# Kernel tuning notes

Hardware: AMD Instinct MI355X
Metric: run time of the kernel (lower is better)

The kernel has to match this reference:

```python
import jax, jax.numpy as jnp
import numpy as np

EMBED_DIM = 1024
NUM_HEADS = 16
HEAD_DIM = EMBED_DIM // NUM_HEADS
SEQ_LEN = 2048
B = 2


def setup_inputs() -> dict:
    key = jax.random.key(0)
    ks = jax.random.split(key, 6)
    x = jax.random.normal(ks[0], (B, SEQ_LEN, EMBED_DIM), dtype=jnp.float32)
    # Linear params (torch Linear: y = x @ W.T + b); store W as [in, out] for einsum
    qkv_w = jax.random.normal(ks[1], (EMBED_DIM, 3 * EMBED_DIM), dtype=jnp.float32) * (EMBED_DIM ** -0.5)
    qkv_b = jnp.zeros((3 * EMBED_DIM,), dtype=jnp.float32)
    proj_w = jax.random.normal(ks[2], (EMBED_DIM, EMBED_DIM), dtype=jnp.float32) * (EMBED_DIM ** -0.5)
    proj_b = jnp.zeros((EMBED_DIM,), dtype=jnp.float32)
    # relative position bias table [2L-1, H], trunc_normal std=0.02 ~ normal*0.02
    bias_table = jax.random.normal(ks[3], (2 * SEQ_LEN - 1, NUM_HEADS), dtype=jnp.float32) * 0.02
    return {"x": x, "qkv_w": qkv_w, "qkv_b": qkv_b, "proj_w": proj_w, "proj_b": proj_b, "bias_table": bias_table}


def _rel_pos_index(L):
    coords = jnp.arange(L)
    return (coords[None, :] - coords[:, None]) + (SEQ_LEN - 1)  # [L, L] int


def reference(x, qkv_w, qkv_b, proj_w, proj_b, bias_table):
    Bsz, L, C = x.shape
    scale = HEAD_DIM ** -0.5
    qkv = x @ qkv_w + qkv_b                               # [B, L, 3C]
    qkv = qkv.reshape(Bsz, L, 3, NUM_HEADS, HEAD_DIM)
    q = jnp.transpose(qkv[:, :, 0], (0, 2, 1, 3))          # [B, H, L, D]
    k = jnp.transpose(qkv[:, :, 1], (0, 2, 1, 3))
    v = jnp.transpose(qkv[:, :, 2], (0, 2, 1, 3))
    attn = jnp.einsum('bhqd,bhkd->bhqk', q, k) * scale     # [B, H, L, L]
    rel_bias = bias_table[_rel_pos_index(L)]               # [L, L, H]
    attn = attn + jnp.transpose(rel_bias, (2, 0, 1))[None]  # broadcast over batch
    attn = jax.nn.softmax(attn, axis=-1)
    out = jnp.einsum('bhqk,bhkd->bhqd', attn, v)           # [B, H, L, D]
    out = jnp.transpose(out, (0, 2, 1, 3)).reshape(Bsz, L, C)
    return out @ proj_w + proj_b
```

## Files before the change

kernel.cpp:

```cpp
#include <hip/hip_runtime.h>

typedef short bf16x4 __attribute__((ext_vector_type(4)));
typedef short bf16x8 __attribute__((ext_vector_type(8)));
typedef float f32x4 __attribute__((ext_vector_type(4)));
typedef float f32x16 __attribute__((ext_vector_type(16)));

__device__ __forceinline__ unsigned short f2bf(float f) {
  union { float f; unsigned int u; } v; v.f = f;
  unsigned int r = v.u + 0x7FFFu + ((v.u >> 16) & 1u);
  return (unsigned short)(r >> 16);
}

__device__ __forceinline__ float exp2_fast(float x) {
  float r;
  asm("v_exp_f32 %0, %1" : "=v"(r) : "v"(x));
  return r;
}

__device__ __forceinline__ unsigned int cvt_pk_bf16(float lo, float hi) {
  unsigned int r;
  asm("v_cvt_pk_bf16_f32 %0, %1, %2" : "=v"(r) : "v"(lo), "v"(hi));
  return r;
}


__global__ __launch_bounds__(256) void k_convert_x(const float4* __restrict__ in,
                                                   ushort4* __restrict__ out) {
  int id = blockIdx.x * 256 + threadIdx.x;
  float4 v = in[id];
  ushort4 o;
  o.x = f2bf(v.x); o.y = f2bf(v.y); o.z = f2bf(v.z); o.w = f2bf(v.w);
  out[id] = o;
}

__global__ __launch_bounds__(256) void k_transpose_bf16(const float* __restrict__ in,
                                                        unsigned short* __restrict__ out,
                                                        int R, int C) {
  __shared__ float tile[32][33];
  int tx = threadIdx.x, ty = threadIdx.y;
  int c0 = blockIdx.x * 32, r0 = blockIdx.y * 32;
#pragma unroll
  for (int i = 0; i < 32; i += 8) tile[ty + i][tx] = in[(size_t)(r0 + ty + i) * C + c0 + tx];
  __syncthreads();
#pragma unroll
  for (int i = 0; i < 32; i += 8) out[(size_t)(c0 + ty + i) * R + r0 + tx] = f2bf(tile[tx][ty + i]);
}

__global__ __launch_bounds__(256) void k_bias_cols(const float* __restrict__ bt,
                                                   float* __restrict__ bh) {
  int i = blockIdx.x * 256 + threadIdx.x;
  if (i < 4095 * 16) bh[(i & 15) * 4096 + (i >> 4)] = bt[i] * 1.44269504089f;
}

template <int EPI>
__global__ __launch_bounds__(512) void k_gemm(const unsigned short* __restrict__ A,
                                              const unsigned short* __restrict__ Bt,
                                              const float* __restrict__ bias,
                                              float* __restrict__ Cf,
                                              unsigned short* __restrict__ qb,
                                              unsigned short* __restrict__ kb,
                                              unsigned short* __restrict__ vtb) {
  __shared__ unsigned short Alds[2][128 * 64];
  __shared__ unsigned short Blds[2][128 * 64];
  const int t = threadIdx.x;
  const int l = t & 63, w = t >> 6;
  const int l15 = l & 15, l4 = l >> 4;
  const int wm = w >> 2, wn = w & 3;

  const int hwid = blockIdx.x;
  const int x = hwid & 7, loc = hwid >> 3;
  const int bm = ((x >> 1) * 8 + (loc & 7)) * 128;
  const int bn = ((x & 1) * (EPI ? 12 : 4) + (loc >> 3)) * 128;

  const int srow = t >> 3;
  const int sc = t & 7;
  const unsigned short* agl = A + (size_t)(bm + srow) * 1024 + sc * 8;
  const unsigned short* bgl = Bt + (size_t)(bn + srow) * 1024 + sc * 8;
  const int wls = srow * 64 + ((sc ^ (srow & 7)) * 8);

  f32x4 acc[4][2];
#pragma unroll
  for (int i = 0; i < 4; ++i)
#pragma unroll
    for (int j = 0; j < 2; ++j) acc[i][j] = (f32x4){0.f, 0.f, 0.f, 0.f};

  bf16x8 ra[4], rb[4];

#define GLOAD(REGS, KT)                                                       \
  _Pragma("unroll") for (int q = 0; q < 2; ++q) {                             \
    REGS[q] = *(const bf16x8*)(agl + (size_t)q * 65536 + (KT) * 64);          \
    REGS[2 + q] = *(const bf16x8*)(bgl + (size_t)q * 65536 + (KT) * 64);      \
  }
#define SWRITE(REGS, CUR)                                                     \
  _Pragma("unroll") for (int q = 0; q < 2; ++q) {                             \
    *(bf16x8*)&Alds[CUR][q * 4096 + wls] = REGS[q];                           \
    *(bf16x8*)&Blds[CUR][q * 4096 + wls] = REGS[2 + q];                       \
  }

  GLOAD(ra, 0);
  GLOAD(rb, 1);
  SWRITE(ra, 0);
  asm volatile("s_waitcnt lgkmcnt(0)" ::: "memory");
  __builtin_amdgcn_s_barrier();

#define GEMM_PHASE(KT, RFREE, RPEND)                                          \
  {                                                                           \
    const int cur_ = (KT) & 1;                                                \
    if ((KT) + 2 < 16) { GLOAD(RFREE, (KT) + 2); }                            \
    __builtin_amdgcn_s_setprio(1);                                            \
    _Pragma("unroll") for (int kc = 0; kc < 2; ++kc) {                        \
      bf16x8 af[4], bv[2];                                                    \
      _Pragma("unroll") for (int i = 0; i < 4; ++i) {                         \
        int ra_ = wm * 64 + i * 16 + l15;                                     \
        af[i] = *(const bf16x8*)&Alds[cur_][ra_ * 64 +                        \
                                            (((kc * 4 + l4) ^ (l15 & 7))) * 8]; \
      }                                                                       \
      _Pragma("unroll") for (int j = 0; j < 2; ++j) {                         \
        int rb_ = wn * 32 + j * 16 + l15;                                     \
        bv[j] = *(const bf16x8*)&Blds[cur_][rb_ * 64 +                        \
                                            (((kc * 4 + l4) ^ (l15 & 7))) * 8]; \
      }                                                                       \
      _Pragma("unroll") for (int i = 0; i < 4; ++i)                           \
        _Pragma("unroll") for (int jn = 0; jn < 2; ++jn)                      \
          acc[i][jn] =                                                        \
              __builtin_amdgcn_mfma_f32_16x16x32_bf16(af[i], bv[jn],          \
                                                      acc[i][jn], 0, 0, 0);   \
    }                                                                         \
    __builtin_amdgcn_s_setprio(0);                                            \
    if ((KT) + 1 < 16) { SWRITE(RPEND, cur_ ^ 1); }                           \
    asm volatile("s_waitcnt lgkmcnt(0)" ::: "memory");                        \
    __builtin_amdgcn_s_barrier();                                             \
  }

  for (int kt = 0; kt < 16; kt += 2) {
    GEMM_PHASE(kt, ra, rb);
    GEMM_PHASE(kt + 1, rb, ra);
  }
#undef GEMM_PHASE
#undef SWRITE
#undef GLOAD

#pragma unroll
  for (int i = 0; i < 4; ++i) {
#pragma unroll
    for (int jn = 0; jn < 2; ++jn) {
      int n = bn + wn * 32 + jn * 16 + l15;
      float bval = bias[n];
#pragma unroll
      for (int j = 0; j < 4; ++j) {
        int m = bm + wm * 64 + i * 16 + l4 * 4 + j;
        float v = acc[i][jn][j] + bval;
        if (EPI == 0) {
          Cf[(size_t)m * 1024 + n] = v;
        } else {
          int which = n >> 10, hh = (n >> 6) & 15, d = n & 63;
          int bb = m >> 11, pos = m & 2047;
          int bhh = bb * 16 + hh;
          if (which == 0)
            qb[((size_t)bhh * 2048 + pos) * 64 + d] = f2bf(v * 0.18033688f);
          else if (which == 1)
            kb[((size_t)bhh * 2048 + pos) * 64 + d] = f2bf(v);
          else
            vtb[((size_t)bhh * 64 + d) * 2048 + pos] = f2bf(v);
        }
      }
    }
  }
}

__global__ __launch_bounds__(256) void k_attn(const unsigned short* __restrict__ qbuf,
                                              const unsigned short* __restrict__ kbuf,
                                              const unsigned short* __restrict__ vtbuf,
                                              const float* __restrict__ biash,
                                              unsigned short* __restrict__ aout) {
  __shared__ __align__(16) unsigned short Klds[2][64 * 64];
  __shared__ __align__(16) unsigned short Vlds[2][64 * 64];

  const int t = threadIdx.x;
  const int w = t >> 6, l = t & 63;
  const int l31 = l & 31, hi = l >> 5;

  const int bid = blockIdx.x;
  const int swzb = (bid & 7) * 64 + (bid >> 3);
  const int qt = swzb & 15;
  const int bh = swzb >> 4;
  const int h = bh & 15, b = bh >> 4;
  const int qbase = qt * 128;
  const int wq = qbase + w * 32;

  bf16x8 qB[4];
  {
    const unsigned short* qrow = qbuf + ((size_t)bh * 2048 + wq + l31) * 64;
#pragma unroll
    for (int ds = 0; ds < 4; ++ds) qB[ds] = *(const bf16x8*)&qrow[ds * 16 + hi * 8];
  }

  f32x16 O[2];
#pragma unroll
  for (int i = 0; i < 16; ++i) { O[0][i] = 0.f; O[1][i] = 0.f; }
  float m_run = -3e38f, l_run = 0.f;

  const int c0r = t >> 3, c0c = t & 7;
  const unsigned short* kg = kbuf + ((size_t)bh * 2048 + c0r) * 64 + c0c * 8;
  const unsigned short* vg = vtbuf + ((size_t)bh * 64 + c0r) * 2048 + c0c * 8;
  const int wKV = c0r * 64 + ((c0c ^ (c0r & 7)) * 8);

  {
    bf16x8 k0 = *(const bf16x8*)(kg);
    bf16x8 k1 = *(const bf16x8*)(kg + 32 * 64);
    bf16x8 v0 = *(const bf16x8*)(vg);
    bf16x8 v1 = *(const bf16x8*)(vg + 32 * 2048);
    *(bf16x8*)&Klds[0][wKV] = k0;
    *(bf16x8*)&Klds[0][wKV + 2048] = k1;
    *(bf16x8*)&Vlds[0][wKV] = v0;
    *(bf16x8*)&Vlds[0][wKV + 2048] = v1;
  }
  __syncthreads();

  const float* bgl = biash + h * 4096 + 2047 - (wq + l31) + 4 * hi;

  for (int kt = 0; kt < 32; ++kt) {
    const int cur = kt & 1;

    bf16x8 kst0, kst1, vst0, vst1;
    if (kt < 31) {
      const unsigned short* kga = kg + (size_t)(kt + 1) * 4096;
      const unsigned short* vga = vg + (kt + 1) * 64;
      kst0 = *(const bf16x8*)(kga);
      kst1 = *(const bf16x8*)(kga + 32 * 64);
      vst0 = *(const bf16x8*)(vga);
      vst1 = *(const bf16x8*)(vga + 32 * 2048);
    }
    const int kbase = kt * 64;

    f32x4 bq[2][4];
#pragma unroll
    for (int kt2 = 0; kt2 < 2; ++kt2)
#pragma unroll
      for (int g = 0; g < 4; ++g)
        __builtin_memcpy(&bq[kt2][g], &bgl[kbase + 32 * kt2 + 8 * g], 16);

    f32x16 sacc[2];
#pragma unroll
    for (int i = 0; i < 16; ++i) { sacc[0][i] = 0.f; sacc[1][i] = 0.f; }
    __builtin_amdgcn_s_setprio(1);
#pragma unroll
    for (int kt2 = 0; kt2 < 2; ++kt2) {
      int row = kt2 * 32 + l31;
      int rsw = row & 7;
#pragma unroll
      for (int ds = 0; ds < 4; ++ds) {
        bf16x8 ka = *(const bf16x8*)&Klds[cur][row * 64 + (((2 * ds + hi) ^ rsw) * 8)];
        sacc[kt2] = __builtin_amdgcn_mfma_f32_32x32x16_bf16(ka, qB[ds], sacc[kt2], 0, 0, 0);
      }
    }
    __builtin_amdgcn_s_setprio(0);

#pragma unroll
    for (int kt2 = 0; kt2 < 2; ++kt2)
#pragma unroll
      for (int g = 0; g < 4; ++g)
#pragma unroll
        for (int r = 0; r < 4; ++r) sacc[kt2][4 * g + r] += bq[kt2][g][r];

    float mx;
    {
      float q0 = fmaxf(fmaxf(sacc[0][0], sacc[0][1]), fmaxf(sacc[0][2], sacc[0][3]));
      float q1 = fmaxf(fmaxf(sacc[0][4], sacc[0][5]), fmaxf(sacc[0][6], sacc[0][7]));
      float q2 = fmaxf(fmaxf(sacc[0][8], sacc[0][9]), fmaxf(sacc[0][10], sacc[0][11]));
      float q3 = fmaxf(fmaxf(sacc[0][12], sacc[0][13]), fmaxf(sacc[0][14], sacc[0][15]));
      float q4 = fmaxf(fmaxf(sacc[1][0], sacc[1][1]), fmaxf(sacc[1][2], sacc[1][3]));
      float q5 = fmaxf(fmaxf(sacc[1][4], sacc[1][5]), fmaxf(sacc[1][6], sacc[1][7]));
      float q6 = fmaxf(fmaxf(sacc[1][8], sacc[1][9]), fmaxf(sacc[1][10], sacc[1][11]));
      float q7 = fmaxf(fmaxf(sacc[1][12], sacc[1][13]), fmaxf(sacc[1][14], sacc[1][15]));
      mx = fmaxf(fmaxf(fmaxf(q0, q1), fmaxf(q2, q3)), fmaxf(fmaxf(q4, q5), fmaxf(q6, q7)));
      mx = fmaxf(mx, __shfl_xor(mx, 32));
    }

    if (__any(mx > m_run + 8.f)) {
      float mnew = fmaxf(m_run, mx);
      float alpha = exp2_fast(m_run - mnew);
      m_run = mnew;
      l_run *= alpha;
#pragma unroll
      for (int g = 0; g < 4; ++g)
#pragma unroll
        for (int r = 0; r < 4; ++r) {
          float a_lo = __shfl(alpha, 8 * g + r);
          float a_hi = __shfl(alpha, 8 * g + r + 4);
          float aq = hi ? a_hi : a_lo;
          O[0][4 * g + r] *= aq;
          O[1][4 * g + r] *= aq;
        }
    }

#pragma unroll
    for (int kt2 = 0; kt2 < 2; ++kt2)
#pragma unroll
      for (int i = 0; i < 16; ++i) sacc[kt2][i] = exp2_fast(sacc[kt2][i] - m_run);
    {
      float s0 = (sacc[0][0] + sacc[0][1]) + (sacc[0][2] + sacc[0][3]);
      float s1 = (sacc[0][4] + sacc[0][5]) + (sacc[0][6] + sacc[0][7]);
      float s2 = (sacc[0][8] + sacc[0][9]) + (sacc[0][10] + sacc[0][11]);
      float s3 = (sacc[0][12] + sacc[0][13]) + (sacc[0][14] + sacc[0][15]);
      float s4 = (sacc[1][0] + sacc[1][1]) + (sacc[1][2] + sacc[1][3]);
      float s5 = (sacc[1][4] + sacc[1][5]) + (sacc[1][6] + sacc[1][7]);
      float s6 = (sacc[1][8] + sacc[1][9]) + (sacc[1][10] + sacc[1][11]);
      float s7 = (sacc[1][12] + sacc[1][13]) + (sacc[1][14] + sacc[1][15]);
      float rs = ((s0 + s1) + (s2 + s3)) + ((s4 + s5) + (s6 + s7));
      rs += __shfl_xor(rs, 32);
      l_run += rs;
    }

    bf16x8 pa[2][2];
#pragma unroll
    for (int kt2 = 0; kt2 < 2; ++kt2)
#pragma unroll
      for (int mm = 0; mm < 2; ++mm) {
        union { unsigned int u[4]; bf16x8 v; } pk;
        pk.u[0] = cvt_pk_bf16(sacc[kt2][8 * mm + 0], sacc[kt2][8 * mm + 1]);
        pk.u[1] = cvt_pk_bf16(sacc[kt2][8 * mm + 2], sacc[kt2][8 * mm + 3]);
        pk.u[2] = cvt_pk_bf16(sacc[kt2][8 * mm + 4], sacc[kt2][8 * mm + 5]);
        pk.u[3] = cvt_pk_bf16(sacc[kt2][8 * mm + 6], sacc[kt2][8 * mm + 7]);
        pa[kt2][mm] = pk.v;
      }

    __builtin_amdgcn_s_setprio(1);
#pragma unroll
    for (int dt = 0; dt < 2; ++dt) {
      int row = dt * 32 + l31;
      int rsw = row & 7;
#pragma unroll
      for (int kt2 = 0; kt2 < 2; ++kt2)
#pragma unroll
        for (int mm = 0; mm < 2; ++mm) {
          int cA = (4 * kt2 + 2 * mm) ^ rsw;
          int cB = (4 * kt2 + 2 * mm + 1) ^ rsw;
          bf16x4 vlo = *(const bf16x4*)&Vlds[cur][row * 64 + cA * 8 + 4 * hi];
          bf16x4 vhi = *(const bf16x4*)&Vlds[cur][row * 64 + cB * 8 + 4 * hi];
          bf16x8 vb = __builtin_shufflevector(vlo, vhi, 0, 1, 2, 3, 4, 5, 6, 7);
          O[dt] = __builtin_amdgcn_mfma_f32_32x32x16_bf16(pa[kt2][mm], vb, O[dt], 0, 0, 0);
        }
    }
    __builtin_amdgcn_s_setprio(0);

    if (kt < 31) {
      *(bf16x8*)&Klds[cur ^ 1][wKV] = kst0;
      *(bf16x8*)&Klds[cur ^ 1][wKV + 2048] = kst1;
      *(bf16x8*)&Vlds[cur ^ 1][wKV] = vst0;
      *(bf16x8*)&Vlds[cur ^ 1][wKV + 2048] = vst1;
    }
    __syncthreads();
  }

  {
    float linv = 1.f / l_run;
#pragma unroll
    for (int g = 0; g < 4; ++g)
#pragma unroll
      for (int r = 0; r < 4; ++r) {
        float v_lo = __shfl(linv, 8 * g + r);
        float v_hi = __shfl(linv, 8 * g + r + 4);
        float sc = hi ? v_hi : v_lo;
        int q = wq + 8 * g + r + 4 * hi;
        size_t base = ((size_t)b * 2048 + q) * 1024 + h * 64 + l31;
        aout[base] = f2bf(O[0][4 * g + r] * sc);
        aout[base + 32] = f2bf(O[1][4 * g + r] * sc);
      }
  }
}


extern "C" void kernel_launch(void* const* d_in, const int* in_sizes, int n_in,
                              void* d_out, int out_size, void* d_ws, size_t ws_size,
                              hipStream_t stream) {
  const float* x = (const float*)d_in[0];
  const float* qkv_w = (const float*)d_in[1];
  const float* qkv_b = (const float*)d_in[2];
  const float* proj_w = (const float*)d_in[3];
  const float* proj_b = (const float*)d_in[4];
  const float* bias_table = (const float*)d_in[5];
  float* out = (float*)d_out;

  char* ws = (char*)d_ws;
  unsigned short* xb = (unsigned short*)(ws);
  unsigned short* wqkv = (unsigned short*)(ws + (size_t)(8u << 20));
  unsigned short* wproj = (unsigned short*)(ws + (size_t)(14u << 20));
  unsigned short* qb = (unsigned short*)(ws + (size_t)(16u << 20));
  unsigned short* kb = (unsigned short*)(ws + (size_t)(24u << 20));
  unsigned short* vtb = (unsigned short*)(ws + (size_t)(32u << 20));
  float* biash = (float*)(ws + (size_t)(40u << 20));

  unsigned short* attn_out = xb;

  k_convert_x<<<dim3(4096), dim3(256), 0, stream>>>((const float4*)x, (ushort4*)xb);
  k_transpose_bf16<<<dim3(96, 32), dim3(32, 8), 0, stream>>>(qkv_w, wqkv, 1024, 3072);
  k_transpose_bf16<<<dim3(32, 32), dim3(32, 8), 0, stream>>>(proj_w, wproj, 1024, 1024);
  k_bias_cols<<<dim3(256), dim3(256), 0, stream>>>(bias_table, biash);

  k_gemm<1><<<dim3(768), dim3(512), 0, stream>>>(xb, wqkv, qkv_b, nullptr, qb, kb, vtb);
  k_attn<<<dim3(512), dim3(256), 0, stream>>>(qb, kb, vtb, biash, attn_out);
  k_gemm<0><<<dim3(256), dim3(512), 0, stream>>>(attn_out, wproj, proj_b, out, nullptr, nullptr,
                                                 nullptr);
}
```

Measured before the change: 142.9 us.

## Split attention key range across two wave groups and merge via LDS

Each attention block now runs 512 threads. Two groups of four waves each process half of the key sequence for the same 128 query rows, and each group has its own double-buffered K/V tiles in LDS. At the end, group 0 writes its partial O and its running max and sum to LDS, and group 1 rescales and combines them before writing the output. This doubles the waves per block and halves the serial key loop, to improve latency hiding with only 512 blocks. In exchange it doubles LDS use and adds a merge step with an extra barrier.

Measured after the change: 239.2 us. 1.67x slower.

```diff
diff --git a/kernel.cpp b/kernel.cpp
--- a/kernel.cpp
+++ b/kernel.cpp
@@ -168,17 +168,18 @@
   }
 }
 
-__global__ __launch_bounds__(256) void k_attn(const unsigned short* __restrict__ qbuf,
-                                              const unsigned short* __restrict__ kbuf,
-                                              const unsigned short* __restrict__ vtbuf,
-                                              const float* __restrict__ biash,
-                                              unsigned short* __restrict__ aout) {
-  __shared__ __align__(16) unsigned short Klds[2][64 * 64];
-  __shared__ __align__(16) unsigned short Vlds[2][64 * 64];
+__global__ __launch_bounds__(512, 4) void k_attn(const unsigned short* __restrict__ qbuf,
+                                                 const unsigned short* __restrict__ kbuf,
+                                                 const unsigned short* __restrict__ vtbuf,
+                                                 const float* __restrict__ biash,
+                                                 unsigned short* __restrict__ aout) {
+  __shared__ __align__(16) unsigned short Klds[2][2][64 * 64];
+  __shared__ __align__(16) unsigned short Vlds[2][2][64 * 64];
 
   const int t = threadIdx.x;
   const int w = t >> 6, l = t & 63;
   const int l31 = l & 31, hi = l >> 5;
+  const int half = w >> 2, wl = w & 3;
 
   const int bid = blockIdx.x;
   const int swzb = (bid & 7) * 64 + (bid >> 3);
@@ -186,7 +187,7 @@
   const int bh = swzb >> 4;
   const int h = bh & 15, b = bh >> 4;
   const int qbase = qt * 128;
-  const int wq = qbase + w * 32;
+  const int wq = qbase + wl * 32;
 
   bf16x8 qB[4];
   {
@@ -200,9 +201,12 @@
   for (int i = 0; i < 16; ++i) { O[0][i] = 0.f; O[1][i] = 0.f; }
   float m_run = -3e38f, l_run = 0.f;
 
-  const int c0r = t >> 3, c0c = t & 7;
-  const unsigned short* kg = kbuf + ((size_t)bh * 2048 + c0r) * 64 + c0c * 8;
-  const unsigned short* vg = vtbuf + ((size_t)bh * 64 + c0r) * 2048 + c0c * 8;
+  const int t256 = t & 255;
+  const int c0r = t256 >> 3, c0c = t256 & 7;
+  const unsigned short* kg =
+      kbuf + ((size_t)bh * 2048 + half * 1024 + c0r) * 64 + c0c * 8;
+  const unsigned short* vg =
+      vtbuf + ((size_t)bh * 64 + c0r) * 2048 + half * 1024 + c0c * 8;
   const int wKV = c0r * 64 + ((c0c ^ (c0r & 7)) * 8);
 
   {
@@ -210,28 +214,28 @@
     bf16x8 k1 = *(const bf16x8*)(kg + 32 * 64);
     bf16x8 v0 = *(const bf16x8*)(vg);
     bf16x8 v1 = *(const bf16x8*)(vg + 32 * 2048);
-    *(bf16x8*)&Klds[0][wKV] = k0;
-    *(bf16x8*)&Klds[0][wKV + 2048] = k1;
-    *(bf16x8*)&Vlds[0][wKV] = v0;
-    *(bf16x8*)&Vlds[0][wKV + 2048] = v1;
+    *(bf16x8*)&Klds[half][0][wKV] = k0;
+    *(bf16x8*)&Klds[half][0][wKV + 2048] = k1;
+    *(bf16x8*)&Vlds[half][0][wKV] = v0;
+    *(bf16x8*)&Vlds[half][0][wKV + 2048] = v1;
   }
   __syncthreads();
 
   const float* bgl = biash + h * 4096 + 2047 - (wq + l31) + 4 * hi;
 
-  for (int kt = 0; kt < 32; ++kt) {
-    const int cur = kt & 1;
+  for (int ktl = 0; ktl < 16; ++ktl) {
+    const int cur = ktl & 1;
 
     bf16x8 kst0, kst1, vst0, vst1;
-    if (kt < 31) {
-      const unsigned short* kga = kg + (size_t)(kt + 1) * 4096;
-      const unsigned short* vga = vg + (kt + 1) * 64;
+    if (ktl < 15) {
+      const unsigned short* kga = kg + (size_t)(ktl + 1) * 4096;
+      const unsigned short* vga = vg + (ktl + 1) * 64;
       kst0 = *(const bf16x8*)(kga);
       kst1 = *(const bf16x8*)(kga + 32 * 64);
       vst0 = *(const bf16x8*)(vga);
       vst1 = *(const bf16x8*)(vga + 32 * 2048);
     }
-    const int kbase = kt * 64;
+    const int kbase = half * 1024 + ktl * 64;
 
     f32x4 bq[2][4];
 #pragma unroll
@@ -250,7 +254,7 @@
       int rsw = row & 7;
 #pragma unroll
       for (int ds = 0; ds < 4; ++ds) {
-        bf16x8 ka = *(const bf16x8*)&Klds[cur][row * 64 + (((2 * ds + hi) ^ rsw) * 8)];
+        bf16x8 ka = *(const bf16x8*)&Klds[half][cur][row * 64 + (((2 * ds + hi) ^ rsw) * 8)];
         sacc[kt2] = __builtin_amdgcn_mfma_f32_32x32x16_bf16(ka, qB[ds], sacc[kt2], 0, 0, 0);
       }
     }
@@ -336,36 +340,61 @@
         for (int mm = 0; mm < 2; ++mm) {
           int cA = (4 * kt2 + 2 * mm) ^ rsw;
           int cB = (4 * kt2 + 2 * mm + 1) ^ rsw;
-          bf16x4 vlo = *(const bf16x4*)&Vlds[cur][row * 64 + cA * 8 + 4 * hi];
-          bf16x4 vhi = *(const bf16x4*)&Vlds[cur][row * 64 + cB * 8 + 4 * hi];
+          bf16x4 vlo = *(const bf16x4*)&Vlds[half][cur][row * 64 + cA * 8 + 4 * hi];
+          bf16x4 vhi = *(const bf16x4*)&Vlds[half][cur][row * 64 + cB * 8 + 4 * hi];
           bf16x8 vb = __builtin_shufflevector(vlo, vhi, 0, 1, 2, 3, 4, 5, 6, 7);
           O[dt] = __builtin_amdgcn_mfma_f32_32x32x16_bf16(pa[kt2][mm], vb, O[dt], 0, 0, 0);
         }
     }
     __builtin_amdgcn_s_setprio(0);
 
-    if (kt < 31) {
-      *(bf16x8*)&Klds[cur ^ 1][wKV] = kst0;
-      *(bf16x8*)&Klds[cur ^ 1][wKV + 2048] = kst1;
-      *(bf16x8*)&Vlds[cur ^ 1][wKV] = vst0;
-      *(bf16x8*)&Vlds[cur ^ 1][wKV + 2048] = vst1;
+    if (ktl < 15) {
+      *(bf16x8*)&Klds[half][cur ^ 1][wKV] = kst0;
+      *(bf16x8*)&Klds[half][cur ^ 1][wKV + 2048] = kst1;
+      *(bf16x8*)&Vlds[half][cur ^ 1][wKV] = vst0;
+      *(bf16x8*)&Vlds[half][cur ^ 1][wKV + 2048] = vst1;
     }
     __syncthreads();
   }
 
-  {
-    float linv = 1.f / l_run;
+  float* ox = (float*)(&Klds[0][0][0]);
+  float* mlm = (float*)(&Vlds[0][0][0]);
+  if (half == 0) {
 #pragma unroll
     for (int g = 0; g < 4; ++g)
 #pragma unroll
       for (int r = 0; r < 4; ++r) {
-        float v_lo = __shfl(linv, 8 * g + r);
-        float v_hi = __shfl(linv, 8 * g + r + 4);
-        float sc = hi ? v_hi : v_lo;
-        int q = wq + 8 * g + r + 4 * hi;
+        int row = 8 * g + r + 4 * hi;
+        ox[wl * 2048 + row * 64 + l31] = O[0][4 * g + r];
+        ox[wl * 2048 + row * 64 + 32 + l31] = O[1][4 * g + r];
+      }
+    if (hi == 0) {
+      mlm[wl * 32 + l31] = m_run;
+      mlm[128 + wl * 32 + l31] = l_run;
+    }
+  }
+  __syncthreads();
+  if (half == 1) {
+    float ma = mlm[wl * 32 + l31];
+    float la = mlm[128 + wl * 32 + l31];
+    float mc = fmaxf(ma, m_run);
+    float aa = exp2_fast(ma - mc);
+    float ab = exp2_fast(m_run - mc);
+    float linv = 1.f / (la * aa + l_run * ab);
+#pragma unroll
+    for (int g = 0; g < 4; ++g)
+#pragma unroll
+      for (int r = 0; r < 4; ++r) {
+        int xr = 8 * g + r + 4 * hi;
+        float aaX = __shfl(aa, xr);
+        float abX = __shfl(ab, xr);
+        float lvX = __shfl(linv, xr);
+        float vA0 = ox[wl * 2048 + xr * 64 + l31];
+        float vA1 = ox[wl * 2048 + xr * 64 + 32 + l31];
+        int q = wq + xr;
         size_t base = ((size_t)b * 2048 + q) * 1024 + h * 64 + l31;
-        aout[base] = f2bf(O[0][4 * g + r] * sc);
-        aout[base + 32] = f2bf(O[1][4 * g + r] * sc);
+        aout[base] = f2bf((vA0 * aaX + O[0][4 * g + r] * abX) * lvX);
+        aout[base + 32] = f2bf((vA1 * aaX + O[1][4 * g + r] * abX) * lvX);
       }
   }
 }
@@ -399,7 +428,7 @@
   k_bias_cols<<<dim3(256), dim3(256), 0, stream>>>(bias_table, biash);
 
   k_gemm<1><<<dim3(768), dim3(512), 0, stream>>>(xb, wqkv, qkv_b, nullptr, qb, kb, vtb);
-  k_attn<<<dim3(512), dim3(256), 0, stream>>>(qb, kb, vtb, biash, attn_out);
+  k_attn<<<dim3(512), dim3(512), 0, stream>>>(qb, kb, vtb, biash, attn_out);
   k_gemm<0><<<dim3(256), dim3(512), 0, stream>>>(attn_out, wproj, proj_b, out, nullptr, nullptr,
                                                  nullptr);
 }
```
